# Kernel tuning notes

Hardware: AMD Instinct MI355X
Metric: run time of the kernel (lower is better)

Reference implementation:

```python
import jax, jax.numpy as jnp
import numpy as np

N_HEAD, D_K = 16, 64  # from init_kwargs (d_v == d_k)

def setup_inputs() -> dict:
    key = jax.random.key(0)
    ks = jax.random.split(key, 8)
    B, S, D, DFF = 8, 1024, 1024, 4096
    s = 1.0 / np.sqrt(D)
    return {
        "enc_input": jax.random.normal(ks[0], (B, S, D), jnp.float32),
        "mask": jnp.ones((B, 1, S), jnp.int32),
        "gap": 1,
        "wq": jax.random.normal(ks[1], (D, N_HEAD * D_K), jnp.float32) * s,
        "wk": jax.random.normal(ks[2], (D, N_HEAD * D_K), jnp.float32) * s,
        "wv": jax.random.normal(ks[3], (D, N_HEAD * D_K), jnp.float32) * s,
        "wo": jax.random.normal(ks[4], (N_HEAD * D_K, D), jnp.float32) * s,
        "w1": jax.random.normal(ks[5], (D, DFF), jnp.float32) * s,
        "b1": jnp.zeros((DFF,), jnp.float32),
        "w2": jax.random.normal(ks[6], (DFF, D), jnp.float32) * (1.0 / np.sqrt(DFF)),
        "b2": jnp.zeros((D,), jnp.float32),
    }

def reference(enc_input, mask, gap, wq, wk, wv, wo, w1, b1, w2, b2):
    # dropout=0, use_layer_norm=0, adapter=0 are hard-coded in EncoderLayer.__init__
    B, S, D = enc_input.shape
    H, dk = N_HEAD, D_K
    temperature = dk ** 0.5

    q = (enc_input @ wq).reshape(B, S, H, dk).transpose(0, 2, 1, 3)  # [B,H,S,dk]
    k = (enc_input @ wk).reshape(B, S, H, dk).transpose(0, 2, 1, 3)
    v = (enc_input @ wv).reshape(B, S, H, dk).transpose(0, 2, 1, 3)

    attn = jnp.einsum('bhqd,bhkd->bhqk', q / temperature, k)  # [B,H,S,S]
    # mask [B,1,S] -> unsqueeze head dim -> [B,1,1,S]
    attn = jnp.where(mask[:, None] == 0, jnp.float32(-1e9), attn)
    attn = jax.nn.softmax(attn, axis=-1)

    ctx = jnp.einsum('bhqk,bhkd->bhqd', attn, v)          # [B,H,S,dk]
    ctx = ctx.transpose(0, 2, 1, 3).reshape(B, S, H * dk)  # [B,S,D]
    enc = ctx @ wo + enc_input                              # attn residual

    ffn = jax.nn.relu(enc @ w1 + b1) @ w2 + b2
    out = ffn + enc                                         # ffn residual
    return out, attn
```

## Files before the change

### kernel.cpp

```cpp
#include <hip/hip_runtime.h>
#include <hip/hip_bf16.h>
#include <stdint.h>

typedef __bf16 bf16x8 __attribute__((ext_vector_type(8)));
typedef float  f32x4  __attribute__((ext_vector_type(4)));

typedef __attribute__((address_space(1))) void gvoid;
typedef __attribute__((address_space(3))) void lvoid;

__device__ __forceinline__ void async16(void* lds, const void* g) {
    __builtin_amdgcn_global_load_lds((gvoid*)g, (lvoid*)lds, 16, 0, 0);
}

__global__ void cvt_f32_to_bf16(const float* __restrict__ in,
                                __hip_bfloat16* __restrict__ out, long n) {
    long i = ((long)blockIdx.x * blockDim.x + threadIdx.x) * 4;
    if (i < n) {
        float4 v = *(const float4*)(in + i);
        __hip_bfloat162* d = (__hip_bfloat162*)(out + i);
        d[0] = __float22bfloat162_rn(make_float2(v.x, v.y));
        d[1] = __float22bfloat162_rn(make_float2(v.z, v.w));
    }
}

__global__ void prep_weights(const float* __restrict__ wq, const float* __restrict__ wk,
                             const float* __restrict__ wv, const float* __restrict__ wo,
                             const float* __restrict__ w1, const float* __restrict__ w2,
                             __hip_bfloat16* __restrict__ Wcat,
                             __hip_bfloat16* __restrict__ Wot,
                             __hip_bfloat16* __restrict__ W1t,
                             __hip_bfloat16* __restrict__ W2t) {
    __shared__ float t[32][33];
    const int tix = blockIdx.x;
    const float* in;
    __hip_bfloat16* out;
    int R, C, cx, cy;
    if (tix < 4096) {
        int wid = tix >> 10, tile = tix & 1023;
        const float* srcs[4] = {wq, wk, wv, wo};
        __hip_bfloat16* dsts[4] = {Wcat, Wcat + 1024 * 1024, Wcat + 2 * 1024 * 1024, Wot};
        in = srcs[wid]; out = dsts[wid];
        R = 1024; C = 1024; cx = tile & 31; cy = tile >> 5;
    } else if (tix < 8192) {
        int tile = tix - 4096;
        in = w1; out = W1t; R = 1024; C = 4096;
        cx = tile & 127; cy = tile >> 7;
    } else {
        int tile = tix - 8192;
        in = w2; out = W2t; R = 4096; C = 1024;
        cx = tile & 31; cy = tile >> 5;
    }
    const int c0 = cx * 32, r0 = cy * 32;
    const int tx = threadIdx.x, ty = threadIdx.y;
#pragma unroll
    for (int i = 0; i < 4; ++i) {
        int r = r0 + ty + i * 8;
        t[ty + i * 8][tx] = in[(long)r * C + c0 + tx];
    }
    __syncthreads();
#pragma unroll
    for (int i = 0; i < 4; ++i) {
        int c = c0 + ty + i * 8;
        out[(long)c * R + r0 + tx] = __float2bfloat16(t[tx][ty + i * 8]);
    }
}

__global__ void transpose_v(const __hip_bfloat16* __restrict__ QKV,
                            __hip_bfloat16* __restrict__ Vt) {
    __shared__ __hip_bfloat16 t[32][33];
    int s0 = blockIdx.x * 32, d0 = blockIdx.y * 32, z = blockIdx.z;
    int b = z >> 4, h = z & 15;
    int tx = threadIdx.x, ty = threadIdx.y;
#pragma unroll
    for (int i = 0; i < 4; ++i) {
        int s = s0 + ty + i * 8;
        t[ty + i * 8][tx] = QKV[((long)b * 1024 + s) * 3072 + 2048 + h * 64 + d0 + tx];
    }
    __syncthreads();
#pragma unroll
    for (int i = 0; i < 4; ++i) {
        int d = d0 + ty + i * 8;
        Vt[((long)z * 64 + d) * 1024 + s0 + tx] = t[tx][ty + i * 8];
    }
}

__global__ void __launch_bounds__(256, 2)
attn_fused(const __hip_bfloat16* __restrict__ QKV,
           const __hip_bfloat16* __restrict__ Vt,
           const int* __restrict__ mask,
           float* __restrict__ attn,
           __hip_bfloat16* __restrict__ Ctx) {
    __shared__ __align__(16) __hip_bfloat16 sK[128 * 64];
    __shared__ __align__(16) __hip_bfloat16 sV[64 * 128];
    __shared__ __align__(16) __hip_bfloat16 sP[128 * 128];
    __shared__ float smadd[1024];

    const int tid = threadIdx.x, lane = tid & 63, wave = tid >> 6;
    const int r16 = lane & 15, kg = lane >> 4;

    const int dd = blockIdx.x;
    const int wgt = (dd & 7) * 128 + (dd >> 3);
    const int xblk = wgt & 7, z = wgt >> 3;
    const int b = z >> 4, h = z & 15;
    const int row0 = xblk * 128;
    const int wrow = wave * 32;

    const __hip_bfloat16* Qz = QKV + ((long)b * 1024 + row0) * 3072 + h * 64;
    const __hip_bfloat16* Kz = QKV + (long)b * 1024 * 3072 + 1024 + h * 64;
    const __hip_bfloat16* Vz = Vt + (long)z * 64 * 1024;
    float* attnZ = attn + (long)z * 1024 * 1024 + (long)row0 * 1024;

    for (int i = tid; i < 1024; i += 256)
        smadd[i] = mask[b * 1024 + i] ? 0.f : -1e9f;

    bf16x8 qa[2][2];
#pragma unroll
    for (int m = 0; m < 2; ++m)
#pragma unroll
        for (int kf = 0; kf < 2; ++kf)
            qa[m][kf] = *(const bf16x8*)(Qz + (long)(wrow + m * 16 + r16) * 3072 + kf * 32 + kg * 8);

    float lrow[2][4];
#pragma unroll
    for (int m = 0; m < 2; ++m)
#pragma unroll
        for (int i = 0; i < 4; ++i) lrow[m][i] = 0.f;

    const int ssw = (r16 & 7) << 4;

    auto stageK = [&](char* dst, int ct) {
#pragma unroll
        for (int j = 0; j < 4; ++j) {
            int c = wave * 4 + j;
            int s = c * 8 + (lane >> 3);
            int cb = (lane & 7) * 16;
            async16(dst + c * 1024,
                    (const char*)(Kz + (long)(ct * 128 + s) * 3072) + (cb ^ ((s & 7) << 4)));
        }
    };
    auto stageV = [&](int ct) {
#pragma unroll
        for (int j = 0; j < 4; ++j) {
            int c = wave * 4 + j;
            int dv = c * 4 + (lane >> 4);
            int cb = (lane & 15) * 16;
            async16((char*)sV + c * 1024,
                    (const char*)(Vz + (long)dv * 1024 + ct * 128) + (cb ^ ((dv & 7) << 4)));
        }
    };

    char* kbuf0 = (char*)sK;
    char* kbuf1 = (char*)sP;
    stageK(kbuf0, 0);

    for (int ct = 0; ct < 8; ++ct) {
        asm volatile("s_waitcnt vmcnt(0)" ::: "memory");
        __syncthreads();
        if (ct < 7) stageK((ct & 1) ? kbuf0 : kbuf1, ct + 1);
        const char* base = (ct & 1) ? kbuf1 : kbuf0;

        f32x4 sacc[2][8];
#pragma unroll
        for (int m = 0; m < 2; ++m)
#pragma unroll
            for (int nf = 0; nf < 8; ++nf) sacc[m][nf] = f32x4{0.f, 0.f, 0.f, 0.f};

#pragma unroll
        for (int nf = 0; nf < 8; ++nf) {
            const char* kr = base + (nf * 16 + r16) * 128;
            bf16x8 bv0 = *(const bf16x8*)(kr + ((kg * 16) ^ ssw));
            bf16x8 bv1 = *(const bf16x8*)(kr + ((64 + kg * 16) ^ ssw));
#pragma unroll
            for (int m = 0; m < 2; ++m) {
                sacc[m][nf] = __builtin_amdgcn_mfma_f32_16x16x32_bf16(qa[m][0], bv0, sacc[m][nf], 0, 0, 0);
                sacc[m][nf] = __builtin_amdgcn_mfma_f32_16x16x32_bf16(qa[m][1], bv1, sacc[m][nf], 0, 0, 0);
            }
        }

        float madd[8];
#pragma unroll
        for (int nf = 0; nf < 8; ++nf) madd[nf] = smadd[ct * 128 + nf * 16 + r16];

#pragma unroll
        for (int m = 0; m < 2; ++m)
#pragma unroll
            for (int i = 0; i < 4; ++i) {
                float ts = 0.f;
#pragma unroll
                for (int nf = 0; nf < 8; ++nf)
                    ts += __expf(sacc[m][nf][i] * 0.125f + madd[nf]);
#pragma unroll
                for (int o = 1; o < 16; o <<= 1) ts += __shfl_xor(ts, o);
                lrow[m][i] += ts;
            }
    }

    float rinv[2][4];
#pragma unroll
    for (int m = 0; m < 2; ++m)
#pragma unroll
        for (int i = 0; i < 4; ++i) rinv[m][i] = 1.0f / lrow[m][i];

    f32x4 oacc[2][4];
#pragma unroll
    for (int m = 0; m < 2; ++m)
#pragma unroll
        for (int nf = 0; nf < 4; ++nf) oacc[m][nf] = f32x4{0.f, 0.f, 0.f, 0.f};

    __syncthreads();
    stageK((char*)sK, 0);
    stageV(0);

    for (int ct = 0; ct < 8; ++ct) {
        asm volatile("s_waitcnt vmcnt(0)" ::: "memory");
        __syncthreads();

        f32x4 sacc[2][8];
#pragma unroll
        for (int m = 0; m < 2; ++m)
#pragma unroll
            for (int nf = 0; nf < 8; ++nf) sacc[m][nf] = f32x4{0.f, 0.f, 0.f, 0.f};

#pragma unroll
        for (int nf = 0; nf < 8; ++nf) {
            const char* kr = (const char*)sK + (nf * 16 + r16) * 128;
            bf16x8 bv0 = *(const bf16x8*)(kr + ((kg * 16) ^ ssw));
            bf16x8 bv1 = *(const bf16x8*)(kr + ((64 + kg * 16) ^ ssw));
#pragma unroll
            for (int m = 0; m < 2; ++m) {
                sacc[m][nf] = __builtin_amdgcn_mfma_f32_16x16x32_bf16(qa[m][0], bv0, sacc[m][nf], 0, 0, 0);
                sacc[m][nf] = __builtin_amdgcn_mfma_f32_16x16x32_bf16(qa[m][1], bv1, sacc[m][nf], 0, 0, 0);
            }
        }

        __syncthreads();
        if (ct < 7) stageK((char*)sK, ct + 1);

        float madd[8];
#pragma unroll
        for (int nf = 0; nf < 8; ++nf) madd[nf] = smadd[ct * 128 + nf * 16 + r16];

#pragma unroll
        for (int m = 0; m < 2; ++m)
#pragma unroll
            for (int nf = 0; nf < 8; ++nf) {
                int scol = nf * 16 + r16;
#pragma unroll
                for (int i = 0; i < 4; ++i) {
                    int q = wrow + m * 16 + kg * 4 + i;
                    float p = __expf(sacc[m][nf][i] * 0.125f + madd[nf]) * rinv[m][i];
                    attnZ[(long)q * 1024 + ct * 128 + scol] = p;
                    *(__hip_bfloat16*)((char*)sP + q * 256 + ((scol * 2) ^ ((q & 7) << 4))) =
                        __float2bfloat16(p);
                }
            }

#pragma unroll
        for (int ks = 0; ks < 4; ++ks) {
            bf16x8 pa[2], vv[4];
#pragma unroll
            for (int m = 0; m < 2; ++m)
                pa[m] = *(const bf16x8*)((const char*)sP + (wrow + m * 16 + r16) * 256 +
                                         ((ks * 64 + kg * 16) ^ ssw));
#pragma unroll
            for (int nf = 0; nf < 4; ++nf)
                vv[nf] = *(const bf16x8*)((const char*)sV + (nf * 16 + r16) * 256 +
                                          ((ks * 64 + kg * 16) ^ ssw));
#pragma unroll
            for (int m = 0; m < 2; ++m)
#pragma unroll
                for (int nf = 0; nf < 4; ++nf)
                    oacc[m][nf] = __builtin_amdgcn_mfma_f32_16x16x32_bf16(pa[m], vv[nf], oacc[m][nf], 0, 0, 0);
        }

        __syncthreads();
        if (ct < 7) stageV(ct + 1);
    }

#pragma unroll
    for (int m = 0; m < 2; ++m)
#pragma unroll
        for (int nf = 0; nf < 4; ++nf)
#pragma unroll
            for (int i = 0; i < 4; ++i) {
                int q = wrow + m * 16 + kg * 4 + i;
                Ctx[((long)b * 1024 + row0 + q) * 1024 + h * 64 + nf * 16 + r16] =
                    __float2bfloat16(oacc[m][nf][i]);
            }
}

#define RDA(BUF, PM, ML, KS) \
    (*(const bf16x8*)(aRd + (BUF)*32768 + (PM)*16384 + (ML)*2048 + ((((KS)*64) + kg*16) ^ sw)))
#define RDB(BUF, PN, NL, KS) \
    (*(const bf16x8*)(bRd + (BUF)*32768 + (PN)*16384 + (NL)*2048 + ((((KS)*64) + kg*16) ^ sw)))
#define LOAD_A(BUF, PM)                          \
    _Pragma("unroll") for (int ml = 0; ml < 4; ++ml) \
    _Pragma("unroll") for (int ks = 0; ks < 2; ++ks) \
        a[ml][ks] = RDA(BUF, PM, ml, ks)
#define LOAD_B(DST, BUF, PN)                     \
    _Pragma("unroll") for (int nl = 0; nl < 2; ++nl) \
    _Pragma("unroll") for (int ks = 0; ks < 2; ++ks) \
        DST[nl][ks] = RDB(BUF, PN, nl, ks)
#define MFMA16(PM, PN, BB)                                                   \
    __builtin_amdgcn_s_setprio(1);                                           \
    _Pragma("unroll") for (int ks = 0; ks < 2; ++ks)                         \
    _Pragma("unroll") for (int ml = 0; ml < 4; ++ml)                         \
    _Pragma("unroll") for (int nl = 0; nl < 2; ++nl)                         \
        acc[(PM)*4 + ml][(PN)*2 + nl] = __builtin_amdgcn_mfma_f32_16x16x32_bf16( \
            a[ml][ks], BB[nl][ks], acc[(PM)*4 + ml][(PN)*2 + nl], 0, 0, 0);  \
    __builtin_amdgcn_s_setprio(0)
#define BAR asm volatile("s_barrier" ::: "memory")

__global__ void __launch_bounds__(512, 2)
gemm256(const __hip_bfloat16* __restrict__ A, int lda,
        const __hip_bfloat16* __restrict__ Bt, int ldb,
        int K, int Mtiles,
        const float* __restrict__ bias, int relu,
        __hip_bfloat16* __restrict__ C, int ldc) {
    __shared__ __align__(16) char lds[131072];
    const int NT = K >> 6;
    const int tid = threadIdx.x, lane = tid & 63, wave = tid >> 6;
    const int r16 = lane & 15, kg = lane >> 4;
    const int wr = wave >> 2, wc = wave & 3;
    const int sw = (r16 & 7) << 4;

    const int nwg = gridDim.x;
    const int q8 = nwg >> 3, r8 = nwg & 7;
    const int xcd = blockIdx.x & 7, rest = blockIdx.x >> 3;
    const int wg = (xcd < r8 ? xcd * (q8 + 1) : r8 * (q8 + 1) + (xcd - r8) * q8) + rest;
    const int tm = wg % Mtiles, tn = wg / Mtiles;
    const long row0 = (long)tm * 256, col0 = (long)tn * 256;

    const int idx = tid >> 3;
    const int slotp = ((tid & 7) ^ (idx & 7)) * 8;
    const __hip_bfloat16* aSrc[4];
    const __hip_bfloat16* bSrc[4];
#pragma unroll
    for (int j = 0; j < 4; ++j) {
        long ar = row0 + (j & 1) * 128 + (j >> 1) * 64 + idx;
        aSrc[j] = A + ar * lda + slotp;
        long br = col0 + ((j & 1) * 2 + (tid >> 8)) * 64 + (j >> 1) * 32 + (idx & 31);
        bSrc[j] = Bt + br * ldb + slotp;
    }

    char* ldsA = lds;
    char* ldsB = lds + 65536;
    const int stDst = wave * 1024;
    auto stA = [&](int v, int j) {
        async16(ldsA + ((v & 1) << 15) + (j << 13) + stDst, aSrc[j] + (v << 6));
    };
    auto stB = [&](int v, int j) {
        async16(ldsB + ((v & 1) << 15) + (j << 13) + stDst, bSrc[j] + (v << 6));
    };

    stA(0, 0); stA(0, 1); stB(0, 0); stB(0, 1);
    stA(0, 2); stA(0, 3); stB(0, 2); stB(0, 3);
    stA(1, 0); stA(1, 1); stB(1, 0); stB(1, 1);
    asm volatile("s_waitcnt vmcnt(4)" ::: "memory");
    BAR;

    f32x4 acc[8][4] = {};
    const char* aRd = ldsA + wr * 8192 + r16 * 128;
    const char* bRd = ldsB + wc * 4096 + r16 * 128;

    for (int u = 0; u < NT; u += 2) {
        const bool more = (u + 2) < NT;
        bf16x8 a[4][2], b0[2][2], b1[2][2];

        LOAD_A(0, 0);
        LOAD_B(b0, 0, 0);
        stA(u + 1, 2); stA(u + 1, 3);
        MFMA16(0, 0, b0);
        BAR;

        LOAD_B(b1, 0, 1);
        stB(u + 1, 2); stB(u + 1, 3);
        MFMA16(0, 1, b1);
        BAR;

        LOAD_A(0, 1);
        if (more) { stA(u + 2, 0); stA(u + 2, 1); }
        MFMA16(1, 0, b0);
        BAR;

        if (more) {
            stB(u + 2, 0); stB(u + 2, 1);
            asm volatile("s_waitcnt vmcnt(4)" ::: "memory");
        } else {
            asm volatile("s_waitcnt vmcnt(0)" ::: "memory");
        }
        MFMA16(1, 1, b1);
        BAR;

        LOAD_A(1, 0);
        LOAD_B(b0, 1, 0);
        if (more) { stA(u + 2, 2); stA(u + 2, 3); }
        MFMA16(0, 0, b0);
        BAR;

        LOAD_B(b1, 1, 1);
        if (more) { stB(u + 2, 2); stB(u + 2, 3); }
        MFMA16(0, 1, b1);
        BAR;

        LOAD_A(1, 1);
        if (more) { stA(u + 3, 0); stA(u + 3, 1); }
        MFMA16(1, 0, b0);
        BAR;

        if (more) {
            stB(u + 3, 0); stB(u + 3, 1);
            asm volatile("s_waitcnt vmcnt(4)" ::: "memory");
        }
        MFMA16(1, 1, b1);
        BAR;
    }

    const long crow = row0 + wr * 128, ccol = col0 + wc * 64;
#pragma unroll
    for (int mf = 0; mf < 8; ++mf)
#pragma unroll
        for (int nf = 0; nf < 4; ++nf) {
            const long col = ccol + nf * 16 + r16;
            const float bs = bias ? bias[col] : 0.f;
#pragma unroll
            for (int i = 0; i < 4; ++i) {
                const long row = crow + mf * 16 + kg * 4 + i;
                float v = acc[mf][nf][i] + bs;
                if (relu) v = fmaxf(v, 0.f);
                C[row * (long)ldc + col] = __float2bfloat16(v);
            }
        }
}

#define RDB128(BUF, NL, KS) \
    (*(const bf16x8*)(bRd + (BUF)*16384 + (NL)*2048 + ((((KS)*64) + kg*16) ^ sw)))
#define LOAD_B128(DST, BUF)                      \
    _Pragma("unroll") for (int nl = 0; nl < 2; ++nl) \
    _Pragma("unroll") for (int ks = 0; ks < 2; ++ks) \
        DST[nl][ks] = RDB128(BUF, nl, ks)
#define MFMA16N(PM, BB)                                                      \
    __builtin_amdgcn_s_setprio(1);                                           \
    _Pragma("unroll") for (int ks = 0; ks < 2; ++ks)                         \
    _Pragma("unroll") for (int ml = 0; ml < 4; ++ml)                         \
    _Pragma("unroll") for (int nl = 0; nl < 2; ++nl)                         \
        acc[(PM)*4 + ml][nl] = __builtin_amdgcn_mfma_f32_16x16x32_bf16(      \
            a[ml][ks], BB[nl][ks], acc[(PM)*4 + ml][nl], 0, 0, 0);           \
    __builtin_amdgcn_s_setprio(0)

__global__ void __launch_bounds__(512, 2)
gemm256n128(const __hip_bfloat16* __restrict__ A, int lda,
            const __hip_bfloat16* __restrict__ Bt, int ldb,
            int K, int Mtiles,
            const float* __restrict__ bias, int relu,
            const float* __restrict__ resf,
            const __hip_bfloat16* __restrict__ resb, int ldres,
            float* __restrict__ Cf, __hip_bfloat16* __restrict__ Cb, int ldc) {
    __shared__ __align__(16) char lds[98304];
    const int NT = K >> 6;
    const int tid = threadIdx.x, lane = tid & 63, wave = tid >> 6;
    const int r16 = lane & 15, kg = lane >> 4;
    const int wr = wave >> 2, wc = wave & 3;
    const int sw = (r16 & 7) << 4;

    const int nwg = gridDim.x;
    const int q8 = nwg >> 3, r8 = nwg & 7;
    const int xcd = blockIdx.x & 7, rest = blockIdx.x >> 3;
    const int wg = (xcd < r8 ? xcd * (q8 + 1) : r8 * (q8 + 1) + (xcd - r8) * q8) + rest;
    const int tm = wg % Mtiles, tn = wg / Mtiles;
    const long row0 = (long)tm * 256, col0 = (long)tn * 128;

    const int idx = tid >> 3;
    const int slotp = ((tid & 7) ^ (idx & 7)) * 8;
    const __hip_bfloat16* aSrc[4];
    const __hip_bfloat16* bSrc[2];
#pragma unroll
    for (int j = 0; j < 4; ++j) {
        long ar = row0 + (j & 1) * 128 + (j >> 1) * 64 + idx;
        aSrc[j] = A + ar * lda + slotp;
    }
#pragma unroll
    for (int j = 0; j < 2; ++j) {
        long br = col0 + j * 64 + idx;
        bSrc[j] = Bt + br * ldb + slotp;
    }

    char* ldsA = lds;
    char* ldsB = lds + 65536;
    const int stDst = wave * 1024;
    auto stA = [&](int v, int j) {
        async16(ldsA + ((v & 1) << 15) + (j << 13) + stDst, aSrc[j] + (v << 6));
    };
    auto stB = [&](int v, int j) {
        async16(ldsB + ((v & 1) << 14) + (j << 13) + stDst, bSrc[j] + (v << 6));
    };

    stA(0, 0); stA(0, 1); stA(0, 2); stA(0, 3);
    stB(0, 0); stB(0, 1);
    stA(1, 0); stA(1, 1);
    stB(1, 0); stB(1, 1);
    asm volatile("s_waitcnt vmcnt(4)" ::: "memory");
    BAR;

    f32x4 acc[8][2] = {};
    const char* aRd = ldsA + wr * 8192 + r16 * 128;
    const char* bRd = ldsB + wc * 4096 + r16 * 128;

    for (int u = 0; u < NT; u += 2) {
        const bool more = (u + 2) < NT;
        bf16x8 a[4][2], b0[2][2], b1[2][2];

        LOAD_A(0, 0);
        LOAD_B128(b0, 0);
        stA(u + 1, 2); stA(u + 1, 3);
        MFMA16N(0, b0);
        BAR;

        LOAD_A(0, 1);
        if (more) {
            stA(u + 2, 0); stA(u + 2, 1);
            stB(u + 2, 0); stB(u + 2, 1);
            asm volatile("s_waitcnt vmcnt(4)" ::: "memory");
        } else {
            asm volatile("s_waitcnt vmcnt(0)" ::: "memory");
        }
        MFMA16N(1, b0);
        BAR;

        LOAD_A(1, 0);
        LOAD_B128(b1, 1);
        if (more) { stA(u + 2, 2); stA(u + 2, 3); }
        MFMA16N(0, b1);
        BAR;

        LOAD_A(1, 1);
        if (more) {
            stA(u + 3, 0); stA(u + 3, 1);
            stB(u + 3, 0); stB(u + 3, 1);
            asm volatile("s_waitcnt vmcnt(4)" ::: "memory");
        }
        MFMA16N(1, b1);
        BAR;
    }

    const long crow = row0 + wr * 128, ccol = col0 + wc * 32;
#pragma unroll
    for (int mf = 0; mf < 8; ++mf)
#pragma unroll
        for (int nf = 0; nf < 2; ++nf) {
            const long col = ccol + nf * 16 + r16;
            const float bs = bias ? bias[col] : 0.f;
#pragma unroll
            for (int i = 0; i < 4; ++i) {
                const long row = crow + mf * 16 + kg * 4 + i;
                float v = acc[mf][nf][i] + bs;
                if (relu) v = fmaxf(v, 0.f);
                if (resf) v += resf[row * (long)ldres + col];
                if (resb) v += __bfloat162float(resb[row * (long)ldres + col]);
                const long off = row * (long)ldc + col;
                if (Cf) Cf[off] = v;
                if (Cb) Cb[off] = __float2bfloat16(v);
            }
        }
}

extern "C" void kernel_launch(void* const* d_in, const int* in_sizes, int n_in,
                              void* d_out, int out_size, void* d_ws, size_t ws_size,
                              hipStream_t stream) {
    const int B = 8, S = 1024, D = 1024, DFF = 4096;
    const long SD = (long)B * S * D;

    const float* X  = (const float*)d_in[0];
    const int*  msk = (const int*)d_in[1];
    const float* wq = (const float*)d_in[3];
    const float* wk = (const float*)d_in[4];
    const float* wv = (const float*)d_in[5];
    const float* wo = (const float*)d_in[6];
    const float* w1 = (const float*)d_in[7];
    const float* b1 = (const float*)d_in[8];
    const float* w2 = (const float*)d_in[9];
    const float* b2 = (const float*)d_in[10];

    float* out  = (float*)d_out;
    float* attn = out + SD;

    char* ws = (char*)d_ws;
    auto alloc = [&](size_t bytes) {
        char* p = ws;
        ws += (bytes + 255) & ~(size_t)255;
        return p;
    };
    __hip_bfloat16* Xb   = (__hip_bfloat16*)alloc(SD * 2);
    __hip_bfloat16* QKVb = (__hip_bfloat16*)alloc(SD * 3 * 2);
    __hip_bfloat16* Vt   = (__hip_bfloat16*)alloc(SD * 2);
    __hip_bfloat16* Ctx  = (__hip_bfloat16*)alloc(SD * 2);
    __hip_bfloat16* EncB = (__hip_bfloat16*)alloc(SD * 2);
    __hip_bfloat16* Hb   = (__hip_bfloat16*)alloc((long)B * S * DFF * 2);
    __hip_bfloat16* Wcat = (__hip_bfloat16*)alloc((long)3 * D * D * 2);
    __hip_bfloat16* Wot  = (__hip_bfloat16*)alloc((long)D * D * 2);
    __hip_bfloat16* W1t  = (__hip_bfloat16*)alloc((long)D * DFF * 2);
    __hip_bfloat16* W2t  = (__hip_bfloat16*)alloc((long)D * DFF * 2);
    (void)ws_size; (void)in_sizes; (void)n_in; (void)out_size;

    dim3 tb(32, 8);
    cvt_f32_to_bf16<<<(int)(SD / 4 / 256), 256, 0, stream>>>(X, Xb, SD);
    prep_weights<<<dim3(12288), tb, 0, stream>>>(wq, wk, wv, wo, w1, w2,
                                                 Wcat, Wot, W1t, W2t);

    gemm256<<<dim3(32 * 12), 512, 0, stream>>>(
        Xb, D, Wcat, D, D, 32, nullptr, 0, QKVb, 3 * D);

    transpose_v<<<dim3(32, 2, 128), tb, 0, stream>>>(QKVb, Vt);

    attn_fused<<<dim3(1024), 256, 0, stream>>>(QKVb, Vt, msk, attn, Ctx);

    gemm256n128<<<dim3(32 * 8), 512, 0, stream>>>(
        Ctx, D, Wot, D, D, 32,
        nullptr, 0, X, nullptr, D,
        nullptr, EncB, D);

    gemm256<<<dim3(32 * 16), 512, 0, stream>>>(
        EncB, D, W1t, D, D, 32, b1, 1, Hb, DFF);

    gemm256n128<<<dim3(32 * 8), 512, 0, stream>>>(
        Hb, DFF, W2t, DFF, DFF, 32,
        b2, 0, nullptr, EncB, D,
        out, nullptr, D);
}
```

Baseline: 518.9 us.

## Drop 256x256 GEMM in favor of 256x128 kernel, merge prep kernels, add MFMA priority

Removes the 256x256-tile gemm256 kernel and routes the QKV and FFN1 GEMMs through the 256x128 gemm256n128 kernel, doubling grid size so more workgroups cover the CUs. Merges the input conversion and weight transpose kernels into one launch, and wraps the attention MFMA loops with s_setprio to favor matrix issue. The smaller tiles use less LDS and may allow better occupancy and load balance, at the cost of lower per-tile data reuse and more global traffic.

Result: slower. 564.3 us (+8.8%).

```diff
diff --git a/kernel.cpp b/kernel.cpp
--- a/kernel.cpp
+++ b/kernel.cpp
@@ -12,26 +12,26 @@
     __builtin_amdgcn_global_load_lds((gvoid*)g, (lvoid*)lds, 16, 0, 0);
 }
 
-__global__ void cvt_f32_to_bf16(const float* __restrict__ in,
-                                __hip_bfloat16* __restrict__ out, long n) {
-    long i = ((long)blockIdx.x * blockDim.x + threadIdx.x) * 4;
-    if (i < n) {
-        float4 v = *(const float4*)(in + i);
-        __hip_bfloat162* d = (__hip_bfloat162*)(out + i);
+__global__ void prep_all(const float* __restrict__ X, __hip_bfloat16* __restrict__ Xb,
+                         const float* __restrict__ wq, const float* __restrict__ wk,
+                         const float* __restrict__ wv, const float* __restrict__ wo,
+                         const float* __restrict__ w1, const float* __restrict__ w2,
+                         __hip_bfloat16* __restrict__ Wcat,
+                         __hip_bfloat16* __restrict__ Wot,
+                         __hip_bfloat16* __restrict__ W1t,
+                         __hip_bfloat16* __restrict__ W2t) {
+    const int tix = blockIdx.x;
+    if (tix >= 12288) {
+        const int bi = tix - 12288;
+        const int tid = threadIdx.y * 32 + threadIdx.x;
+        const long i = ((long)bi * 256 + tid) * 4;
+        float4 v = *(const float4*)(X + i);
+        __hip_bfloat162* d = (__hip_bfloat162*)(Xb + i);
         d[0] = __float22bfloat162_rn(make_float2(v.x, v.y));
         d[1] = __float22bfloat162_rn(make_float2(v.z, v.w));
-    }
-}
-
-__global__ void prep_weights(const float* __restrict__ wq, const float* __restrict__ wk,
-                             const float* __restrict__ wv, const float* __restrict__ wo,
-                             const float* __restrict__ w1, const float* __restrict__ w2,
-                             __hip_bfloat16* __restrict__ Wcat,
-                             __hip_bfloat16* __restrict__ Wot,
-                             __hip_bfloat16* __restrict__ W1t,
-                             __hip_bfloat16* __restrict__ W2t) {
+        return;
+    }
     __shared__ float t[32][33];
-    const int tix = blockIdx.x;
     const float* in;
     __hip_bfloat16* out;
     int R, C, cx, cy;
@@ -165,6 +165,7 @@
 #pragma unroll
             for (int nf = 0; nf < 8; ++nf) sacc[m][nf] = f32x4{0.f, 0.f, 0.f, 0.f};
 
+        __builtin_amdgcn_s_setprio(1);
 #pragma unroll
         for (int nf = 0; nf < 8; ++nf) {
             const char* kr = base + (nf * 16 + r16) * 128;
@@ -176,6 +177,7 @@
                 sacc[m][nf] = __builtin_amdgcn_mfma_f32_16x16x32_bf16(qa[m][1], bv1, sacc[m][nf], 0, 0, 0);
             }
         }
+        __builtin_amdgcn_s_setprio(0);
 
         float madd[8];
 #pragma unroll
@@ -221,6 +223,7 @@
 #pragma unroll
             for (int nf = 0; nf < 8; ++nf) sacc[m][nf] = f32x4{0.f, 0.f, 0.f, 0.f};
 
+        __builtin_amdgcn_s_setprio(1);
 #pragma unroll
         for (int nf = 0; nf < 8; ++nf) {
             const char* kr = (const char*)sK + (nf * 16 + r16) * 128;
@@ -232,6 +235,7 @@
                 sacc[m][nf] = __builtin_amdgcn_mfma_f32_16x16x32_bf16(qa[m][1], bv1, sacc[m][nf], 0, 0, 0);
             }
         }
+        __builtin_amdgcn_s_setprio(0);
 
         __syncthreads();
         if (ct < 7) stageK((char*)sK, ct + 1);
@@ -255,6 +259,7 @@
                 }
             }
 
+        __builtin_amdgcn_s_setprio(1);
 #pragma unroll
         for (int ks = 0; ks < 4; ++ks) {
             bf16x8 pa[2], vv[4];
@@ -272,6 +277,7 @@
                 for (int nf = 0; nf < 4; ++nf)
                     oacc[m][nf] = __builtin_amdgcn_mfma_f32_16x16x32_bf16(pa[m], vv[nf], oacc[m][nf], 0, 0, 0);
         }
+        __builtin_amdgcn_s_setprio(0);
 
         __syncthreads();
         if (ct < 7) stageV(ct + 1);
@@ -289,156 +295,16 @@
             }
 }
 
-#define RDA(BUF, PM, ML, KS) \
-    (*(const bf16x8*)(aRd + (BUF)*32768 + (PM)*16384 + (ML)*2048 + ((((KS)*64) + kg*16) ^ sw)))
-#define RDB(BUF, PN, NL, KS) \
-    (*(const bf16x8*)(bRd + (BUF)*32768 + (PN)*16384 + (NL)*2048 + ((((KS)*64) + kg*16) ^ sw)))
-#define LOAD_A(BUF, PM)                          \
+#define LOAD_A(BUF, PM)                              \
     _Pragma("unroll") for (int ml = 0; ml < 4; ++ml) \
     _Pragma("unroll") for (int ks = 0; ks < 2; ++ks) \
-        a[ml][ks] = RDA(BUF, PM, ml, ks)
-#define LOAD_B(DST, BUF, PN)                     \
+        a[ml][ks] = *(const bf16x8*)(aRd + (BUF)*32768 + (PM)*16384 + ml*2048 + \
+                                     (((ks*64) + kg*16) ^ sw))
+#define LOAD_B128(DST, BUF)                          \
     _Pragma("unroll") for (int nl = 0; nl < 2; ++nl) \
     _Pragma("unroll") for (int ks = 0; ks < 2; ++ks) \
-        DST[nl][ks] = RDB(BUF, PN, nl, ks)
-#define MFMA16(PM, PN, BB)                                                   \
-    __builtin_amdgcn_s_setprio(1);                                           \
-    _Pragma("unroll") for (int ks = 0; ks < 2; ++ks)                         \
-    _Pragma("unroll") for (int ml = 0; ml < 4; ++ml)                         \
-    _Pragma("unroll") for (int nl = 0; nl < 2; ++nl)                         \
-        acc[(PM)*4 + ml][(PN)*2 + nl] = __builtin_amdgcn_mfma_f32_16x16x32_bf16( \
-            a[ml][ks], BB[nl][ks], acc[(PM)*4 + ml][(PN)*2 + nl], 0, 0, 0);  \
-    __builtin_amdgcn_s_setprio(0)
-#define BAR asm volatile("s_barrier" ::: "memory")
-
-__global__ void __launch_bounds__(512, 2)
-gemm256(const __hip_bfloat16* __restrict__ A, int lda,
-        const __hip_bfloat16* __restrict__ Bt, int ldb,
-        int K, int Mtiles,
-        const float* __restrict__ bias, int relu,
-        __hip_bfloat16* __restrict__ C, int ldc) {
-    __shared__ __align__(16) char lds[131072];
-    const int NT = K >> 6;
-    const int tid = threadIdx.x, lane = tid & 63, wave = tid >> 6;
-    const int r16 = lane & 15, kg = lane >> 4;
-    const int wr = wave >> 2, wc = wave & 3;
-    const int sw = (r16 & 7) << 4;
-
-    const int nwg = gridDim.x;
-    const int q8 = nwg >> 3, r8 = nwg & 7;
-    const int xcd = blockIdx.x & 7, rest = blockIdx.x >> 3;
-    const int wg = (xcd < r8 ? xcd * (q8 + 1) : r8 * (q8 + 1) + (xcd - r8) * q8) + rest;
-    const int tm = wg % Mtiles, tn = wg / Mtiles;
-    const long row0 = (long)tm * 256, col0 = (long)tn * 256;
-
-    const int idx = tid >> 3;
-    const int slotp = ((tid & 7) ^ (idx & 7)) * 8;
-    const __hip_bfloat16* aSrc[4];
-    const __hip_bfloat16* bSrc[4];
-#pragma unroll
-    for (int j = 0; j < 4; ++j) {
-        long ar = row0 + (j & 1) * 128 + (j >> 1) * 64 + idx;
-        aSrc[j] = A + ar * lda + slotp;
-        long br = col0 + ((j & 1) * 2 + (tid >> 8)) * 64 + (j >> 1) * 32 + (idx & 31);
-        bSrc[j] = Bt + br * ldb + slotp;
-    }
-
-    char* ldsA = lds;
-    char* ldsB = lds + 65536;
-    const int stDst = wave * 1024;
-    auto stA = [&](int v, int j) {
-        async16(ldsA + ((v & 1) << 15) + (j << 13) + stDst, aSrc[j] + (v << 6));
-    };
-    auto stB = [&](int v, int j) {
-        async16(ldsB + ((v & 1) << 15) + (j << 13) + stDst, bSrc[j] + (v << 6));
-    };
-
-    stA(0, 0); stA(0, 1); stB(0, 0); stB(0, 1);
-    stA(0, 2); stA(0, 3); stB(0, 2); stB(0, 3);
-    stA(1, 0); stA(1, 1); stB(1, 0); stB(1, 1);
-    asm volatile("s_waitcnt vmcnt(4)" ::: "memory");
-    BAR;
-
-    f32x4 acc[8][4] = {};
-    const char* aRd = ldsA + wr * 8192 + r16 * 128;
-    const char* bRd = ldsB + wc * 4096 + r16 * 128;
-
-    for (int u = 0; u < NT; u += 2) {
-        const bool more = (u + 2) < NT;
-        bf16x8 a[4][2], b0[2][2], b1[2][2];
-
-        LOAD_A(0, 0);
-        LOAD_B(b0, 0, 0);
-        stA(u + 1, 2); stA(u + 1, 3);
-        MFMA16(0, 0, b0);
-        BAR;
-
-        LOAD_B(b1, 0, 1);
-        stB(u + 1, 2); stB(u + 1, 3);
-        MFMA16(0, 1, b1);
-        BAR;
-
-        LOAD_A(0, 1);
-        if (more) { stA(u + 2, 0); stA(u + 2, 1); }
-        MFMA16(1, 0, b0);
-        BAR;
-
-        if (more) {
-            stB(u + 2, 0); stB(u + 2, 1);
-            asm volatile("s_waitcnt vmcnt(4)" ::: "memory");
-        } else {
-            asm volatile("s_waitcnt vmcnt(0)" ::: "memory");
-        }
-        MFMA16(1, 1, b1);
-        BAR;
-
-        LOAD_A(1, 0);
-        LOAD_B(b0, 1, 0);
-        if (more) { stA(u + 2, 2); stA(u + 2, 3); }
-        MFMA16(0, 0, b0);
-        BAR;
-
-        LOAD_B(b1, 1, 1);
-        if (more) { stB(u + 2, 2); stB(u + 2, 3); }
-        MFMA16(0, 1, b1);
-        BAR;
-
-        LOAD_A(1, 1);
-        if (more) { stA(u + 3, 0); stA(u + 3, 1); }
-        MFMA16(1, 0, b0);
-        BAR;
-
-        if (more) {
-            stB(u + 3, 0); stB(u + 3, 1);
-            asm volatile("s_waitcnt vmcnt(4)" ::: "memory");
-        }
-        MFMA16(1, 1, b1);
-        BAR;
-    }
-
-    const long crow = row0 + wr * 128, ccol = col0 + wc * 64;
-#pragma unroll
-    for (int mf = 0; mf < 8; ++mf)
-#pragma unroll
-        for (int nf = 0; nf < 4; ++nf) {
-            const long col = ccol + nf * 16 + r16;
-            const float bs = bias ? bias[col] : 0.f;
-#pragma unroll
-            for (int i = 0; i < 4; ++i) {
-                const long row = crow + mf * 16 + kg * 4 + i;
-                float v = acc[mf][nf][i] + bs;
-                if (relu) v = fmaxf(v, 0.f);
-                C[row * (long)ldc + col] = __float2bfloat16(v);
-            }
-        }
-}
-
-#define RDB128(BUF, NL, KS) \
-    (*(const bf16x8*)(bRd + (BUF)*16384 + (NL)*2048 + ((((KS)*64) + kg*16) ^ sw)))
-#define LOAD_B128(DST, BUF)                      \
-    _Pragma("unroll") for (int nl = 0; nl < 2; ++nl) \
-    _Pragma("unroll") for (int ks = 0; ks < 2; ++ks) \
-        DST[nl][ks] = RDB128(BUF, nl, ks)
+        DST[nl][ks] = *(const bf16x8*)(bRd + (BUF)*16384 + nl*2048 + \
+                                       (((ks*64) + kg*16) ^ sw))
 #define MFMA16N(PM, BB)                                                      \
     __builtin_amdgcn_s_setprio(1);                                           \
     _Pragma("unroll") for (int ks = 0; ks < 2; ++ks)                         \
@@ -447,6 +313,7 @@
         acc[(PM)*4 + ml][nl] = __builtin_amdgcn_mfma_f32_16x16x32_bf16(      \
             a[ml][ks], BB[nl][ks], acc[(PM)*4 + ml][nl], 0, 0, 0);           \
     __builtin_amdgcn_s_setprio(0)
+#define BAR asm volatile("s_barrier" ::: "memory")
 
 __global__ void __launch_bounds__(512, 2)
 gemm256n128(const __hip_bfloat16* __restrict__ A, int lda,
@@ -603,12 +470,13 @@
     (void)ws_size; (void)in_sizes; (void)n_in; (void)out_size;
 
     dim3 tb(32, 8);
-    cvt_f32_to_bf16<<<(int)(SD / 4 / 256), 256, 0, stream>>>(X, Xb, SD);
-    prep_weights<<<dim3(12288), tb, 0, stream>>>(wq, wk, wv, wo, w1, w2,
-                                                 Wcat, Wot, W1t, W2t);
-
-    gemm256<<<dim3(32 * 12), 512, 0, stream>>>(
-        Xb, D, Wcat, D, D, 32, nullptr, 0, QKVb, 3 * D);
+    prep_all<<<dim3(12288 + 8192), tb, 0, stream>>>(X, Xb, wq, wk, wv, wo, w1, w2,
+                                                    Wcat, Wot, W1t, W2t);
+
+    gemm256n128<<<dim3(32 * 24), 512, 0, stream>>>(
+        Xb, D, Wcat, D, D, 32,
+        nullptr, 0, nullptr, nullptr, 0,
+        nullptr, QKVb, 3 * D);
 
     transpose_v<<<dim3(32, 2, 128), tb, 0, stream>>>(QKVb, Vt);
 
@@ -619,8 +487,10 @@
         nullptr, 0, X, nullptr, D,
         nullptr, EncB, D);
 
-    gemm256<<<dim3(32 * 16), 512, 0, stream>>>(
-        EncB, D, W1t, D, D, 32, b1, 1, Hb, DFF);
+    gemm256n128<<<dim3(32 * 32), 512, 0, stream>>>(
+        EncB, D, W1t, D, D, 32,
+        b1, 1, nullptr, nullptr, 0,
+        nullptr, Hb, DFF);
 
     gemm256n128<<<dim3(32 * 8), 512, 0, stream>>>(
         Hb, DFF, W2t, DFF, DFF, 32,
```
